# Optimization experiments

Measured on AMD Instinct MI355X. Metric: run time of the kernel, lower is better.

Reference implementation:

```python
import jax, jax.numpy as jnp
from jax import lax
import numpy as np

MS = 128            # local_map_size
HALF = MS // 2
B, S = 8, 64
C, H, W = 3, 1024, 1024


def setup_inputs() -> dict:
    key = jax.random.key(0)
    ks = jax.random.split(key, 48)
    r = lambda i, shape, s: jax.random.normal(ks[i], shape, jnp.float32) * s
    z = lambda *shape: jnp.zeros(shape, jnp.float32)
    o = lambda *shape: jnp.ones(shape, jnp.float32)
    return {
        "full_map": jax.random.normal(ks[0], (B, C, H, W), jnp.float32),
        "conditions": jax.random.uniform(ks[1], (B, 5), jnp.float32, 0.0, 1024.0),
        "input_seq": jax.random.uniform(ks[2], (B, S, 2), jnp.float32, 0.0, 1024.0),
        "steps_remaining": jax.random.uniform(ks[3], (B, S), jnp.float32, 0.0, 500.0),
        # LocalMapEncoder convs (OIHW) + batchnorm affine params
        "cw1": r(4, (16, 3, 3, 3), 0.2),   "cb1": z(16),  "g1": o(16),  "be1": z(16),
        "cw2": r(5, (32, 16, 3, 3), 0.1),  "cb2": z(32),  "g2": o(32),  "be2": z(32),
        "cw3": r(6, (64, 32, 3, 3), 0.07), "cb3": z(64),  "g3": o(64),  "be3": z(64),
        "cw4": r(7, (128, 64, 3, 3), 0.05),"cb4": z(128), "g4": o(128), "be4": z(128),
        "fw1": r(8, (512, 128 * 8 * 8), 0.01), "fb1": z(512),
        "fw2": r(9, (256, 512), 0.04),         "fb2": z(256),
        # ConditionEncoder (6 -> 128 -> 64)
        "ew1": r(10, (128, 6), 0.05),  "eb1": z(128),
        "ew2": r(11, (64, 128), 0.05), "eb2": z(64),
        # coord embedder (2 -> 32)
        "mw": r(12, (32, 2), 0.05), "mb": z(32),
        # 2-layer LSTM, torch gate order (i, f, g, o)
        "w_ih0": r(13, (4 * 256, 32), 0.05),  "w_hh0": r(14, (4 * 256, 256), 0.05),
        "b_ih0": z(4 * 256), "b_hh0": z(4 * 256),
        "w_ih1": r(15, (4 * 256, 256), 0.05), "w_hh1": r(16, (4 * 256, 256), 0.05),
        "b_ih1": z(4 * 256), "b_hh1": z(4 * 256),
        # context layer (256+256+64=576 -> 128 -> 64) and output (64 -> 2)
        "xw1": r(17, (128, 576), 0.04), "xb1": z(128),
        "xw2": r(18, (64, 128), 0.05),  "xb2": z(64),
        "ow": r(19, (2, 64), 0.1),      "ob": z(2),
    }


def _conv_bn_relu(x, w, b, g, be):
    # stride-2 3x3 conv, padding 1, NCHW/OIHW; BatchNorm in training mode (batch stats)
    y = lax.conv_general_dilated(x, w, (2, 2), ((1, 1), (1, 1)),
                                 dimension_numbers=("NCHW", "OIHW", "NCHW"))
    y = y + b[None, :, None, None]
    mu = y.mean((0, 2, 3), keepdims=True)
    var = y.var((0, 2, 3), keepdims=True)
    y = (y - mu) * lax.rsqrt(var + 1e-5) * g[None, :, None, None] + be[None, :, None, None]
    return jax.nn.relu(y)


def _lstm_layer(x, w_ih, w_hh, b_ih, b_hh):
    # x: [B, S, D] -> hidden states [B, S, Hd]
    bsz, hd = x.shape[0], w_hh.shape[1]
    bias = b_ih + b_hh
    def step(carry, xt):
        h, c = carry
        zg = xt @ w_ih.T + h @ w_hh.T + bias
        i, f, gg, oo = jnp.split(zg, 4, axis=-1)
        c = jax.nn.sigmoid(f) * c + jax.nn.sigmoid(i) * jnp.tanh(gg)
        h = jax.nn.sigmoid(oo) * jnp.tanh(c)
        return (h, c), h
    h0 = jnp.zeros((bsz, hd), x.dtype)
    _, hs = lax.scan(step, (h0, h0), x.transpose(1, 0, 2))
    return hs.transpose(1, 0, 2)


def reference(full_map, conditions, input_seq, steps_remaining,
              cw1, cb1, g1, be1, cw2, cb2, g2, be2,
              cw3, cb3, g3, be3, cw4, cb4, g4, be4,
              fw1, fb1, fw2, fb2, ew1, eb1, ew2, eb2, mw, mb,
              w_ih0, w_hh0, b_ih0, b_hh0, w_ih1, w_hh1, b_ih1, b_hh1,
              xw1, xb1, xw2, xb2, ow, ob):
    bsz, seq, _ = input_seq.shape
    # --- batched crop+pad gather (replaces host numpy loop): zero-pad map by
    # HALF on each side, then every crop is a dynamic_slice of size MS at (y, x).
    padded = jnp.pad(full_map, ((0, 0), (0, 0), (HALF, HALF), (HALF, HALF)))
    ys = input_seq[..., 0].astype(jnp.int32).reshape(-1)
    xs = input_seq[..., 1].astype(jnp.int32).reshape(-1)
    bidx = jnp.repeat(jnp.arange(bsz, dtype=jnp.int32), seq)
    crop_one = lambda b, y, x: lax.dynamic_slice(padded, (b, 0, y, x), (1, C, MS, MS))[0]
    crops = jax.vmap(crop_one)(bidx, ys, xs)              # [B*S, C, MS, MS]
    # --- LocalMapEncoder
    h = _conv_bn_relu(crops, cw1, cb1, g1, be1)
    h = _conv_bn_relu(h, cw2, cb2, g2, be2)
    h = _conv_bn_relu(h, cw3, cb3, g3, be3)
    h = _conv_bn_relu(h, cw4, cb4, g4, be4)               # [B*S, 128, 8, 8]
    h = h.reshape(h.shape[0], -1)
    h = jax.nn.relu(h @ fw1.T + fb1) @ fw2.T + fb2
    map_features = h.reshape(bsz, seq, -1)                # [B, S, 256]
    # --- ConditionEncoder on [conditions ++ steps_remaining]
    enh = jnp.concatenate(
        [jnp.broadcast_to(conditions[:, None, :], (bsz, seq, 5)),
         steps_remaining[..., None]], axis=-1)            # [B, S, 6]
    cond_features = jax.nn.relu(enh @ ew1.T + eb1) @ ew2.T + eb2  # [B, S, 64]
    # --- route predictor
    emb = jax.nn.relu(input_seq @ mw.T + mb)              # [B, S, 32]
    lstm_out = _lstm_layer(emb, w_ih0, w_hh0, b_ih0, b_hh0)
    lstm_out = _lstm_layer(lstm_out, w_ih1, w_hh1, b_ih1, b_hh1)  # [B, S, 256]
    combined = jnp.concatenate([lstm_out, map_features, cond_features], axis=-1)
    ctx = jax.nn.relu(jax.nn.relu(combined @ xw1.T + xb1) @ xw2.T + xb2)
    return ctx @ ow.T + ob                                # [B, S, 2]
```

## Files before the change

### kernel.cpp

```cpp
#include <hip/hip_runtime.h>

#define TPB 256
#define NLB 64

typedef float f32x4 __attribute__((ext_vector_type(4)));
typedef short bf16x8 __attribute__((ext_vector_type(8)));
typedef unsigned long long u64;

__device__ __forceinline__ float bf2f(unsigned short u) {
  union { unsigned int i; float f; } x; x.i = ((unsigned int)u) << 16; return x.f;
}
__device__ __forceinline__ unsigned short f2bf(float v) {
  union { float f; unsigned int i; } x; x.f = v;
  unsigned int r = (x.i + 0x7fffu + ((x.i >> 16) & 1u)) >> 16;
  return (unsigned short)r;
}
__device__ __forceinline__ float sigf(float x) { return 1.f / (1.f + __expf(-x)); }
__device__ __forceinline__ bf16x8 lda_bf8(const unsigned short* p) {
  union { uint4 u; bf16x8 v; } t; t.u = *(const uint4*)p; return t.v;
}
__device__ __forceinline__ bf16x8 frag_of(const unsigned int* w) {
  union { unsigned int u[4]; bf16x8 v; } t;
  t.u[0] = w[0]; t.u[1] = w[1]; t.u[2] = w[2]; t.u[3] = w[3]; return t.v;
}
__device__ __forceinline__ uint4 bnpack(uint4 v, const float* sst) {
  unsigned int d[4] = {v.x, v.y, v.z, v.w};
  uint4 o; unsigned int* op = (unsigned int*)&o;
#pragma unroll
  for (int t = 0; t < 4; ++t) {
    float a = fmaxf(fmaf(bf2f((unsigned short)(d[t] & 0xffff)), sst[4 * t], sst[4 * t + 1]), 0.f);
    float b = fmaxf(fmaf(bf2f((unsigned short)(d[t] >> 16)), sst[4 * t + 2], sst[4 * t + 3]), 0.f);
    op[t] = (unsigned int)f2bf(a) | ((unsigned int)f2bf(b) << 16);
  }
  return o;
}

__device__ void lstm_seg(int blkid, int p0, int p1, int first,
    const float* __restrict__ iseq, const float* __restrict__ mw, const float* __restrict__ mb,
    const float* __restrict__ w_ih0, const float* __restrict__ w_hh0,
    const float* __restrict__ b_ih0, const float* __restrict__ b_hh0,
    const float* __restrict__ w_ih1, const float* __restrict__ w_hh1,
    const float* __restrict__ b_ih1, const float* __restrict__ b_hh1,
    u64* __restrict__ h0x, u64* __restrict__ h1x,
    float* __restrict__ comb, float* __restrict__ xzg, float* __restrict__ cst,
    char* sm) {
  const int tid = threadIdx.x;
  const int u0 = blkid * 4;
  float (*xz)[8][16] = (float (*)[8][16])sm;
  char* reg2 = sm + 32768;
  float* bias1s = (float*)(sm + 51712);

  float (*embc)[8][32] = (float (*)[8][32])reg2;
  float* mwmb = (float*)(reg2 + 16384);
  unsigned short (*v0s)[264] = (unsigned short (*)[264])reg2;
  unsigned short (*w1h)[264] = (unsigned short (*)[264])(reg2 + 8448);
  float (*P0)[16]  = (float (*)[16])(reg2 + 16896);
  float (*P1a)[16] = (float (*)[16])(reg2 + 17408);
  float (*P1b)[16] = (float (*)[16])(reg2 + 17920);

  const int wv = tid >> 6, lane = tid & 63, fr = lane & 15, kg = lane >> 4;
  const int r = tid & 15, ks = tid >> 4;
  const int R  = (r >> 2) * 256 + u0 + (r & 3);
  const int Rf = (fr >> 2) * 256 + u0 + (fr & 3);

  unsigned int wfrag[8][4];
  {
    const float* wsrc = (wv == 0) ? w_hh0 : (wv == 1) ? w_ih1 : w_hh1;
#pragma unroll
    for (int ch = 0; ch < 8; ++ch)
#pragma unroll
      for (int d = 0; d < 4; ++d) {
        float lo = wsrc[(size_t)Rf * 256 + ch * 32 + kg * 8 + d * 2];
        float hi = wsrc[(size_t)Rf * 256 + ch * 32 + kg * 8 + d * 2 + 1];
        wfrag[ch][d] = (unsigned)f2bf(lo) | ((unsigned)f2bf(hi) << 16);
      }
  }
  if (tid < 16) bias1s[tid] = b_ih1[R] + b_hh1[R];

  if (first) {
    float wtmp[32];
#pragma unroll
    for (int i = 0; i < 32; ++i) wtmp[i] = w_ih0[R * 32 + i];
    const float bias0r = b_ih0[R] + b_hh0[R];
    if (tid < 96) mwmb[tid] = (tid < 64) ? mw[tid] : mb[tid - 64];
    __syncthreads();
    for (int chunk = 0; chunk < 4; ++chunk) {
      if (tid < 128) {
        int pp = tid >> 3, b = tid & 7;
        int pg = chunk * 16 + pp;
        float s0 = iseq[(b * 64 + pg) * 2 + 0];
        float s1 = iseq[(b * 64 + pg) * 2 + 1];
        for (int k = 0; k < 32; ++k)
          embc[pp][b][k] = fmaxf(fmaf(mwmb[2 * k], s0, fmaf(mwmb[2 * k + 1], s1, mwmb[64 + k])), 0.f);
      }
      __syncthreads();
      {
        int pg = chunk * 16 + ks;
        for (int b = 0; b < 8; ++b) {
          float a = bias0r;
          const float* e = &embc[ks][b][0];
#pragma unroll
          for (int k = 0; k < 32; ++k) a = fmaf(wtmp[k], e[k], a);
          xz[pg][b][r] = a;
        }
      }
      __syncthreads();
    }
    for (int i = tid; i < 8192; i += TPB)
      xzg[(size_t)blkid * 8192 + i] = ((float*)xz)[i];
  } else {
    __syncthreads();
    for (int i = tid; i < 8192; i += TPB)
      ((float*)xz)[i] = xzg[(size_t)blkid * 8192 + i];
  }
  __syncthreads();

  for (int i = tid; i < 8 * 264; i += TPB) {
    v0s[8 + i / 264][i % 264] = 0;
    w1h[8 + i / 264][i % 264] = 0;
  }
  float c0 = 0.f, c1 = 0.f;
  if (!first) {
    if (tid < 32) c0 = cst[blkid * 64 + tid];
    else if (tid < 64) c1 = cst[blkid * 64 + tid];
  }
  __syncthreads();

  for (int p = p0; p < p1; ++p) {
    if (tid < 128) {
      if (p >= 1) {
        const unsigned tag0 = (unsigned)p;
        const u64* s0p = &h0x[(size_t)(p - 1) * 1024 + tid * 8];
        u64 e[8];
        for (;;) {
          bool ok = true;
#pragma unroll
          for (int i = 0; i < 8; ++i) {
            e[i] = __hip_atomic_load(&s0p[i], __ATOMIC_RELAXED, __HIP_MEMORY_SCOPE_AGENT);
            ok &= ((unsigned)(e[i] >> 32) == tag0);
          }
          if (ok) break;
          __builtin_amdgcn_s_sleep(1);
        }
#pragma unroll
        for (int i = 0; i < 8; ++i) {
          int g = tid * 8 + i;
          int bb = (g >> 1) & 7, ub = (g >> 4) * 4 + (g & 1) * 2;
          *(unsigned int*)&v0s[bb][ub] = (unsigned int)e[i];
        }
      } else {
#pragma unroll
        for (int i = 0; i < 8; ++i) {
          int g = tid * 8 + i;
          int bb = (g >> 1) & 7, ub = (g >> 4) * 4 + (g & 1) * 2;
          *(unsigned int*)&v0s[bb][ub] = 0u;
        }
      }
    } else {
      int t2 = tid - 128;
      if (p >= 2) {
        const unsigned tag1 = (unsigned)(p - 1);
        const u64* s1p = &h1x[(size_t)(p - 2) * 1024 + t2 * 8];
        u64 e[8];
        for (;;) {
          bool ok = true;
#pragma unroll
          for (int i = 0; i < 8; ++i) {
            e[i] = __hip_atomic_load(&s1p[i], __ATOMIC_RELAXED, __HIP_MEMORY_SCOPE_AGENT);
            ok &= ((unsigned)(e[i] >> 32) == tag1);
          }
          if (ok) break;
          __builtin_amdgcn_s_sleep(1);
        }
#pragma unroll
        for (int i = 0; i < 8; ++i) {
          int g = t2 * 8 + i;
          int bb = (g >> 1) & 7, ub = (g >> 4) * 4 + (g & 1) * 2;
          *(unsigned int*)&w1h[bb][ub] = (unsigned int)e[i];
        }
      } else {
#pragma unroll
        for (int i = 0; i < 8; ++i) {
          int g = t2 * 8 + i;
          int bb = (g >> 1) & 7, ub = (g >> 4) * 4 + (g & 1) * 2;
          *(unsigned int*)&w1h[bb][ub] = 0u;
        }
      }
    }
    __syncthreads();

    if (wv == 0) {
      if (p < 64) {
        f32x4 acc = {0.f, 0.f, 0.f, 0.f};
#pragma unroll
        for (int ch = 0; ch < 8; ++ch) {
          bf16x8 af = lda_bf8(&v0s[fr][ch * 32 + kg * 8]);
          acc = __builtin_amdgcn_mfma_f32_16x16x32_bf16(af, frag_of(wfrag[ch]), acc, 0, 0, 0);
        }
#pragma unroll
        for (int j = 0; j < 4; ++j) {
          int bb2 = (lane >> 4) * 4 + j;
          if (bb2 < 8) P0[bb2][fr] = acc[j];
        }
      }
    } else if (wv == 1) {
      if (p >= 1) {
        f32x4 acc = {0.f, 0.f, 0.f, 0.f};
#pragma unroll
        for (int ch = 0; ch < 8; ++ch) {
          bf16x8 af = lda_bf8(&v0s[fr][ch * 32 + kg * 8]);
          acc = __builtin_amdgcn_mfma_f32_16x16x32_bf16(af, frag_of(wfrag[ch]), acc, 0, 0, 0);
        }
#pragma unroll
        for (int j = 0; j < 4; ++j) {
          int bb2 = (lane >> 4) * 4 + j;
          if (bb2 < 8) P1a[bb2][fr] = acc[j];
        }
      }
    } else if (wv == 2) {
      if (p >= 1) {
        f32x4 acc = {0.f, 0.f, 0.f, 0.f};
#pragma unroll
        for (int ch = 0; ch < 8; ++ch) {
          bf16x8 af = lda_bf8(&w1h[fr][ch * 32 + kg * 8]);
          acc = __builtin_amdgcn_mfma_f32_16x16x32_bf16(af, frag_of(wfrag[ch]), acc, 0, 0, 0);
        }
#pragma unroll
        for (int j = 0; j < 4; ++j) {
          int bb2 = (lane >> 4) * 4 + j;
          if (bb2 < 8) P1b[bb2][fr] = acc[j];
        }
      }
    }
    __syncthreads();

    if (tid < 32 && p < 64) {
      int b = tid >> 2, uu = tid & 3;
      float zi = P0[b][uu]      + xz[p][b][uu];
      float zf = P0[b][4 + uu]  + xz[p][b][4 + uu];
      float zg = P0[b][8 + uu]  + xz[p][b][8 + uu];
      float zo = P0[b][12 + uu] + xz[p][b][12 + uu];
      c0 = sigf(zf) * c0 + sigf(zi) * tanhf(zg);
      float h = sigf(zo) * tanhf(c0);
      float hp = __shfl_xor(h, 1);
      if (!(uu & 1)) {
        unsigned int d = (unsigned int)f2bf(h) | ((unsigned int)f2bf(hp) << 16);
        u64 v = ((u64)(unsigned)(p + 1) << 32) | d;
        __hip_atomic_store(&h0x[(size_t)p * 1024 + blkid * 16 + b * 2 + (uu >> 1)], v,
                           __ATOMIC_RELAXED, __HIP_MEMORY_SCOPE_AGENT);
      }
    } else if (tid >= 32 && tid < 64 && p >= 1) {
      int t2 = tid - 32, b = t2 >> 2, uu = t2 & 3;
      float zi = P1a[b][uu]      + P1b[b][uu]      + bias1s[uu];
      float zf = P1a[b][4 + uu]  + P1b[b][4 + uu]  + bias1s[4 + uu];
      float zg = P1a[b][8 + uu]  + P1b[b][8 + uu]  + bias1s[8 + uu];
      float zo = P1a[b][12 + uu] + P1b[b][12 + uu] + bias1s[12 + uu];
      c1 = sigf(zf) * c1 + sigf(zi) * tanhf(zg);
      float h = sigf(zo) * tanhf(c1);
      comb[(size_t)(b * 64 + (p - 1)) * 576 + u0 + uu] = h;
      float hp = __shfl_xor(h, 1);
      if (!(uu & 1)) {
        unsigned int d = (unsigned int)f2bf(h) | ((unsigned int)f2bf(hp) << 16);
        u64 v = ((u64)(unsigned)p << 32) | d;
        __hip_atomic_store(&h1x[(size_t)(p - 1) * 1024 + blkid * 16 + b * 2 + (uu >> 1)], v,
                           __ATOMIC_RELAXED, __HIP_MEMORY_SCOPE_AGENT);
      }
    }
  }

  if (tid < 32) cst[blkid * 64 + tid] = c0;
  else if (tid < 64) cst[blkid * 64 + tid] = c1;
}

#define LSTM_ARGS const float* __restrict__ iseq_l, const float* __restrict__ mw, const float* __restrict__ mb, \
    const float* __restrict__ w_ih0, const float* __restrict__ w_hh0, \
    const float* __restrict__ b_ih0, const float* __restrict__ b_hh0, \
    const float* __restrict__ w_ih1, const float* __restrict__ w_hh1, \
    const float* __restrict__ b_ih1, const float* __restrict__ b_hh1, \
    u64* __restrict__ h0x, u64* __restrict__ h1x, float* __restrict__ comb, \
    float* __restrict__ xzg, float* __restrict__ cst, int p0, int p1, int first
#define LSTM_PASS(blk) lstm_seg(blk, p0, p1, first, iseq_l, mw, mb, w_ih0, w_hh0, b_ih0, b_hh0, \
    w_ih1, w_hh1, b_ih1, b_hh1, h0x, h1x, comb, xzg, cst, sm)

__global__ __launch_bounds__(TPB, 2) void k_conv1(
    const float* __restrict__ fmap, const float* __restrict__ iseq,
    const unsigned short* __restrict__ wT, const float* __restrict__ bias,
    unsigned short* __restrict__ out, float* __restrict__ part, LSTM_ARGS) {
  __shared__ __align__(16) char sm[52288];
  const int tid = threadIdx.x;
  if (blockIdx.x < NLB) { LSTM_PASS(blockIdx.x); return; }
  const int bidc = blockIdx.x - NLB;
  unsigned short (*patch)[132][8] = (unsigned short (*)[132][8])sm;
  unsigned short (*Bsm)[104] = (unsigned short (*)[104])(sm + 35904);
  float* bs = (float*)(sm + 39232);
  float* swsum = (float*)(sm + 39296);
  float* swsq  = (float*)(sm + 39552);

  const int n = bidc >> 3, R0 = (bidc & 7) << 3;
  const int y = (int)iseq[n * 2], x = (int)iseq[n * 2 + 1];
  const int bimg = n >> 6;

  for (int e = tid; e < 1536; e += TPB) Bsm[e / 96][e % 96] = wT[e];
  if (tid < 16) bs[tid] = bias[tid];
  for (int e = tid; e < 17 * 132; e += TPB)
    *(uint4*)&patch[e / 132][e % 132][0] = uint4{0u, 0u, 0u, 0u};
  __syncthreads();
  for (int e = tid; e < 3 * 17 * 132; e += TPB) {
    int ic = e / 2244, rem = e % 2244, l = rem / 132, c = rem % 132;
    int i = 2 * R0 - 1 + l, j = c - 1;
    float v = 0.f;
    if ((unsigned)i < 128u && (unsigned)j < 128u) {
      int r = y + i - 64, cc = x + j - 64;
      if ((unsigned)r < 1024u && (unsigned)cc < 1024u)
        v = fmap[(((size_t)bimg * 3 + ic) << 20) + ((size_t)r << 10) + cc];
    }
    patch[l][c][ic] = f2bf(v);
  }
  __syncthreads();

  const int w = tid >> 6, lane = tid & 63, fr = lane & 15, kg = lane >> 4;
  f32x4 acc[8];
#pragma unroll
  for (int m = 0; m < 8; ++m) acc[m] = {0.f, 0.f, 0.f, 0.f};
#pragma unroll
  for (int ch = 0; ch < 3; ++ch) {
    int k8 = ch * 4 + kg;
    int ki = (k8 >= 9) ? 0 : ((k8 * 11) >> 5);
    int kj = (k8 >= 9) ? 0 : (k8 - 3 * ki);
    bf16x8 bfr = lda_bf8(&Bsm[fr][k8 * 8]);
#pragma unroll
    for (int m = 0; m < 8; ++m) {
      int p = w * 128 + m * 16 + fr;
      int pr = p >> 6, pc = p & 63;
      bf16x8 af = lda_bf8(&patch[2 * pr + ki][2 * pc + kj][0]);
      acc[m] = __builtin_amdgcn_mfma_f32_16x16x32_bf16(af, bfr, acc[m], 0, 0, 0);
    }
  }
  const int rg = lane >> 4;
  float bb = bs[fr];
  float sps = 0.f, spq = 0.f;
#pragma unroll
  for (int m = 0; m < 8; ++m) {
#pragma unroll
    for (int r = 0; r < 4; ++r) {
      int p = w * 128 + m * 16 + rg * 4 + r;
      int pr = p >> 6, pc = p & 63;
      float v = acc[m][r] + bb;
      sps += v; spq = fmaf(v, v, spq);
      out[(((size_t)n * 64 + R0 + pr) * 64 + pc) * 16 + fr] = f2bf(v);
    }
  }
  sps += __shfl_xor(sps, 16); spq += __shfl_xor(spq, 16);
  sps += __shfl_xor(sps, 32); spq += __shfl_xor(spq, 32);
  if (lane < 16) { swsum[w * 16 + fr] = sps; swsq[w * 16 + fr] = spq; }
  __syncthreads();
  if (tid < 16) {
    float s = swsum[tid] + swsum[16 + tid] + swsum[32 + tid] + swsum[48 + tid];
    float q = swsq[tid] + swsq[16 + tid] + swsq[32 + tid] + swsq[48 + tid];
    part[(size_t)bidc * 32 + tid * 2] = s;
    part[(size_t)bidc * 32 + tid * 2 + 1] = q;
  }
}

template<int CIN, int CB, int NS, int HIN, int HOUT>
__global__ __launch_bounds__(TPB, 2) void k_conv(
    const unsigned short* __restrict__ inb, const float* __restrict__ ssx,
    const unsigned short* __restrict__ wT, const float* __restrict__ bias,
    unsigned short* __restrict__ out, float* __restrict__ part, LSTM_ARGS) {
  constexpr int K = CIN * 9;
  constexpr int K8 = K / 8;
  constexpr int NCH = (K8 + 3) / 4;
  constexpr int KPAD = NCH * 32;
  constexpr int BS = KPAD + 8;
  constexpr int CINP = CIN + 8;
  constexpr int ICG_SH = (CIN == 16) ? 1 : (CIN == 32) ? 2 : 3;
  constexpr int TPR = HOUT / 8;
  constexpr int NT = CB / 16;
  constexpr int COUT_TOT = CB * NS;
  constexpr int PB = 289 * CINP * 2;
  constexpr int BB = CB * BS * 2;
  constexpr int CONVSM = PB + BB + CIN * 8 + CB * 32;
  constexpr int SMSZ = CONVSM > 52288 ? CONVSM : 52288;
  __shared__ __align__(16) char sm[SMSZ];
  const int tid = threadIdx.x;
  if (blockIdx.x < NLB) { LSTM_PASS(blockIdx.x); return; }
  const int bidc = blockIdx.x - NLB;

  unsigned short* patch = (unsigned short*)sm;
  unsigned short* Bsm = (unsigned short*)(sm + PB);
  float* ssl = (float*)(sm + PB + BB);
  float* swsum = (float*)(sm + PB + BB + CIN * 8);
  float* swsq = swsum + 4 * CB;

  const int n = bidc / ((TPR * TPR) * NS);
  const int rem = bidc % ((TPR * TPR) * NS);
  const int tile = rem / NS;
  const int split = rem % NS;
  const int TR0 = (tile / TPR) * 8, TC0 = (tile % TPR) * 8;
  const int oc0 = split * CB;

  for (int i = tid; i < CIN * 2; i += TPB) ssl[i] = ssx[i];
  __syncthreads();

  for (int e = tid; e < 289 * (CIN / 8); e += TPB) {
    int icg = e % (CIN / 8), pix = e / (CIN / 8);
    int row = pix / 17, col = pix % 17;
    int ir = 2 * TR0 - 1 + row, jc = 2 * TC0 - 1 + col;
    uint4 o = {0u, 0u, 0u, 0u};
    if ((unsigned)ir < (unsigned)HIN && (unsigned)jc < (unsigned)HIN) {
      uint4 v = *(const uint4*)&inb[(((size_t)n * HIN + ir) * HIN + jc) * CIN + icg * 8];
      unsigned int d[4] = {v.x, v.y, v.z, v.w};
      unsigned int* op = (unsigned int*)&o;
#pragma unroll
      for (int t = 0; t < 4; ++t) {
        int c = icg * 8 + 2 * t;
        float a = fmaxf(fmaf(bf2f((unsigned short)(d[t] & 0xffff)), ssl[2 * c], ssl[2 * c + 1]), 0.f);
        float b = fmaxf(fmaf(bf2f((unsigned short)(d[t] >> 16)), ssl[2 * c + 2], ssl[2 * c + 3]), 0.f);
        op[t] = (unsigned int)f2bf(a) | ((unsigned int)f2bf(b) << 16);
      }
    }
    *(uint4*)&patch[pix * CINP + icg * 8] = o;
  }
  for (int e = tid; e < CB * (KPAD / 8); e += TPB) {
    int oc = e / (KPAD / 8), k8i = e % (KPAD / 8);
    uint4 v = {0u, 0u, 0u, 0u};
    if (k8i * 8 < K) v = *(const uint4*)&wT[(size_t)(oc0 + oc) * K + k8i * 8];
    *(uint4*)&Bsm[oc * BS + k8i * 8] = v;
  }
  __syncthreads();

  const int wave = tid >> 6, lane = tid & 63;
  const int fr = lane & 15, kg = lane >> 4;
  const int p = wave * 16 + fr;
  const int pr = p >> 3, pc = p & 7;
  f32x4 acc[NT];
#pragma unroll
  for (int j = 0; j < NT; ++j) acc[j] = {0.f, 0.f, 0.f, 0.f};

#pragma unroll
  for (int ch = 0; ch < NCH; ++ch) {
    int k8 = ch * 4 + kg;
    int tap = k8 >> ICG_SH, icg = k8 & ((1 << ICG_SH) - 1);
    int ki = (tap * 11) >> 5;
    int kj = tap - 3 * ki;
    int addr = ((2 * pr + ki) * 17 + (2 * pc + kj)) * CINP + icg * 8;
    if (tap >= 9) addr = 0;
    bf16x8 af = lda_bf8(&patch[addr]);
#pragma unroll
    for (int j = 0; j < NT; ++j) {
      bf16x8 bfr = lda_bf8(&Bsm[(j * 16 + fr) * BS + ch * 32 + kg * 8]);
      acc[j] = __builtin_amdgcn_mfma_f32_16x16x32_bf16(af, bfr, acc[j], 0, 0, 0);
    }
  }
  const int rg = lane >> 4;
#pragma unroll
  for (int j = 0; j < NT; ++j) {
    int oc = oc0 + j * 16 + fr;
    float bb = bias[oc];
    float s1 = 0.f, q1 = 0.f;
#pragma unroll
    for (int r = 0; r < 4; ++r) {
      int pp = wave * 16 + rg * 4 + r;
      int orow = TR0 + (pp >> 3), ocol = TC0 + (pp & 7);
      float v = acc[j][r] + bb;
      s1 += v; q1 = fmaf(v, v, q1);
      out[(((size_t)n * HOUT + orow) * HOUT + ocol) * COUT_TOT + oc] = f2bf(v);
    }
    s1 += __shfl_xor(s1, 16); q1 += __shfl_xor(q1, 16);
    s1 += __shfl_xor(s1, 32); q1 += __shfl_xor(q1, 32);
    if (lane < 16) { swsum[wave * CB + j * 16 + fr] = s1; swsq[wave * CB + j * 16 + fr] = q1; }
  }
  __syncthreads();
  if (tid < CB) {
    float s = swsum[tid] + swsum[CB + tid] + swsum[2 * CB + tid] + swsum[3 * CB + tid];
    float q = swsq[tid] + swsq[CB + tid] + swsq[2 * CB + tid] + swsq[3 * CB + tid];
    part[(size_t)bidc * CB * 2 + tid * 2] = s;
    part[(size_t)bidc * CB * 2 + tid * 2 + 1] = q;
  }
}

__global__ __launch_bounds__(TPB, 2) void k_fc1(
    const unsigned short* __restrict__ A, const unsigned short* __restrict__ W,
    const float* __restrict__ ssx, const float* __restrict__ bias, float* __restrict__ out,
    LSTM_ARGS) {
  __shared__ __align__(16) char sm[52288];
  const int tid = threadIdx.x;
  if (blockIdx.x < NLB) { LSTM_PASS(blockIdx.x); return; }
  const int cid = blockIdx.x - NLB;
  const int bm = (cid >> 3) * 64, bn = (cid & 7) * 64;

  unsigned short (*As)[64] = (unsigned short (*)[64])sm;
  unsigned short (*Bs)[64] = (unsigned short (*)[64])(sm + 8192);
  float* ssl = (float*)(sm + 16384);
  const int lane = tid & 63, wave = tid >> 6;
  const int wr = (wave >> 1) * 32, wc = (wave & 1) * 32;
  f32x4 acc00 = {0.f, 0.f, 0.f, 0.f}, acc01 = acc00, acc10 = acc00, acc11 = acc00;
  const int r0 = tid >> 3, c0 = tid & 7;
  const int fr = lane & 15, kg = lane >> 4;
  for (int i = tid; i < 256; i += TPB) ssl[i] = ssx[i];
  __syncthreads();
  for (int kt = 0; kt < 128; ++kt) {
    const int kb = kt * 64;
    uint4 av0 = *(const uint4*)&A[(size_t)(bm + r0) * 8192 + kb + c0 * 8];
    uint4 av1 = *(const uint4*)&A[(size_t)(bm + r0 + 32) * 8192 + kb + c0 * 8];
    uint4 bv0 = *(const uint4*)&W[(size_t)(bn + r0) * 8192 + kb + c0 * 8];
    uint4 bv1 = *(const uint4*)&W[(size_t)(bn + r0 + 32) * 8192 + kb + c0 * 8];
    const float* sst = &ssl[2 * ((kb + c0 * 8) & 127)];
    __syncthreads();
    av0 = bnpack(av0, sst);
    av1 = bnpack(av1, sst);
    *(uint4*)&As[r0][(c0 ^ (r0 & 7)) * 8] = av0;
    *(uint4*)&As[r0 + 32][(c0 ^ (r0 & 7)) * 8] = av1;
    *(uint4*)&Bs[r0][(c0 ^ (r0 & 7)) * 8] = bv0;
    *(uint4*)&Bs[r0 + 32][(c0 ^ (r0 & 7)) * 8] = bv1;
    __syncthreads();
#pragma unroll
    for (int ks = 0; ks < 2; ++ks) {
      int ch = ks * 4 + kg;
      int ra0 = wr + fr, ra1 = wr + 16 + fr;
      int rb0 = wc + fr, rb1 = wc + 16 + fr;
      bf16x8 a_0 = lda_bf8(&As[ra0][(ch ^ (ra0 & 7)) * 8]);
      bf16x8 a_1 = lda_bf8(&As[ra1][(ch ^ (ra1 & 7)) * 8]);
      bf16x8 b_0 = lda_bf8(&Bs[rb0][(ch ^ (rb0 & 7)) * 8]);
      bf16x8 b_1 = lda_bf8(&Bs[rb1][(ch ^ (rb1 & 7)) * 8]);
      acc00 = __builtin_amdgcn_mfma_f32_16x16x32_bf16(a_0, b_0, acc00, 0, 0, 0);
      acc01 = __builtin_amdgcn_mfma_f32_16x16x32_bf16(a_0, b_1, acc01, 0, 0, 0);
      acc10 = __builtin_amdgcn_mfma_f32_16x16x32_bf16(a_1, b_0, acc10, 0, 0, 0);
      acc11 = __builtin_amdgcn_mfma_f32_16x16x32_bf16(a_1, b_1, acc11, 0, 0, 0);
    }
  }
  const int rg = lane >> 4;
  int n0 = bn + wc + fr, n1 = n0 + 16;
  float bi0 = bias[n0], bi1 = bias[n1];
#pragma unroll
  for (int r = 0; r < 4; ++r) {
    int m0 = bm + wr + rg * 4 + r, m1 = m0 + 16;
    out[m0 * 512 + n0] = fmaxf(acc00[r] + bi0, 0.f);
    out[m0 * 512 + n1] = fmaxf(acc01[r] + bi1, 0.f);
    out[m1 * 512 + n0] = fmaxf(acc10[r] + bi0, 0.f);
    out[m1 * 512 + n1] = fmaxf(acc11[r] + bi1, 0.f);
  }
}

__global__ __launch_bounds__(TPB) void stats_final3(const float* __restrict__ part,
    const float* __restrict__ gamma, const float* __restrict__ beta,
    float* __restrict__ ss, float inv_count, int COUT_BLK, int NSPLIT, int NBID) {
  const int c = blockIdx.x, tid = threadIdx.x;
  const int split = c / COUT_BLK, loc = c % COUT_BLK;
  const int NG = NBID / NSPLIT;
  float s = 0.f, q = 0.f;
  for (int g = tid; g < NG; g += TPB) {
    size_t b = (size_t)g * NSPLIT + split;
    s += part[b * COUT_BLK * 2 + loc * 2];
    q += part[b * COUT_BLK * 2 + loc * 2 + 1];
  }
  __shared__ float rs[TPB], rq[TPB];
  rs[tid] = s; rq[tid] = q;
  __syncthreads();
  for (int off = TPB / 2; off > 0; off >>= 1) {
    if (tid < off) { rs[tid] += rs[tid + off]; rq[tid] += rq[tid + off]; }
    __syncthreads();
  }
  if (tid == 0) {
    float mean = rs[0] * inv_count;
    float var  = rq[0] * inv_count - mean * mean;
    float rstd = rsqrtf(var + 1e-5f);
    float scl  = gamma[c] * rstd;
    ss[2 * c] = scl;
    ss[2 * c + 1] = beta[c] - mean * scl;
  }
}

__global__ __launch_bounds__(TPB) void prep_wt(
    const float* __restrict__ w1, const float* __restrict__ w2,
    const float* __restrict__ w3, const float* __restrict__ w4,
    unsigned short* __restrict__ wt1, unsigned short* __restrict__ wt2,
    unsigned short* __restrict__ wt3, unsigned short* __restrict__ wt4) {
  int i = blockIdx.x * TPB + threadIdx.x;
  if (i < 1536) {
    int oc = i / 96, k = i % 96;
    int tap = k >> 3, ic = k & 7;
    float v = (tap < 9 && ic < 3) ? w1[(oc * 3 + ic) * 9 + tap] : 0.f;
    wt1[i] = f2bf(v);
  } else if (i < 6144) {
    int j = i - 1536;
    int oc = j / 144, k = j % 144;
    wt2[j] = f2bf(w2[(oc * 16 + (k & 15)) * 9 + (k >> 4)]);
  } else if (i < 24576) {
    int j = i - 6144;
    int oc = j / 288, k = j % 288;
    wt3[j] = f2bf(w3[(oc * 32 + (k & 31)) * 9 + (k >> 5)]);
  } else if (i < 98304) {
    int j = i - 24576;
    int oc = j / 576, k = j % 576;
    wt4[j] = f2bf(w4[(oc * 64 + (k & 63)) * 9 + (k >> 6)]);
  }
}

__global__ __launch_bounds__(TPB) void permute_fw1(const float* __restrict__ in,
    unsigned short* __restrict__ out) {
  __shared__ unsigned short l[128 * 66];
  int n = blockIdx.x;
  for (int e = threadIdx.x; e < 8192; e += TPB) {
    int c = e >> 6, pix = e & 63;
    l[c * 66 + pix] = f2bf(in[(size_t)n * 8192 + e]);
  }
  __syncthreads();
  for (int e = threadIdx.x; e < 8192; e += TPB) {
    int pix = e >> 7, c = e & 127;
    out[(size_t)n * 8192 + e] = l[c * 66 + pix];
  }
}

__global__ __launch_bounds__(TPB, 2) void gemm_m64(
    const float* __restrict__ A, const float* __restrict__ W,
    const float* __restrict__ bias, float* __restrict__ out,
    int N, int K, int relu, int ldo, int coff) {
  __shared__ unsigned short As[64 * 40];
  __shared__ unsigned short Bs[64 * 40];
  const int tid = threadIdx.x, lane = tid & 63, wave = tid >> 6;
  const int wr = (wave >> 1) * 32, wc = (wave & 1) * 32;
  const int bm = blockIdx.y * 64, bn = blockIdx.x * 64;
  const int fr = lane & 15, kg = lane >> 4;
  const int sr = tid >> 2, sc = (tid & 3) * 8;
  f32x4 a00 = {0.f, 0.f, 0.f, 0.f}, a01 = a00, a10 = a00, a11 = a00;
  int nch = (K + 31) >> 5;
  for (int ch = 0; ch < nch; ++ch) {
    int kb = ch * 32;
    __syncthreads();
    {
      unsigned short tmp[8];
#pragma unroll
      for (int j = 0; j < 8; ++j) {
        int k = kb + sc + j;
        tmp[j] = (k < K) ? f2bf(A[(size_t)(bm + sr) * K + k]) : (unsigned short)0;
      }
      *(uint4*)&As[sr * 40 + sc] = *(const uint4*)tmp;
      int wrow = bn + sr;
#pragma unroll
      for (int j = 0; j < 8; ++j) {
        int k = kb + sc + j;
        tmp[j] = (wrow < N && k < K) ? f2bf(W[(size_t)wrow * K + k]) : (unsigned short)0;
      }
      *(uint4*)&Bs[sr * 40 + sc] = *(const uint4*)tmp;
    }
    __syncthreads();
    bf16x8 af0 = lda_bf8(&As[(wr + fr) * 40 + kg * 8]);
    bf16x8 af1 = lda_bf8(&As[(wr + 16 + fr) * 40 + kg * 8]);
    bf16x8 bf0 = lda_bf8(&Bs[(wc + fr) * 40 + kg * 8]);
    bf16x8 bf1 = lda_bf8(&Bs[(wc + 16 + fr) * 40 + kg * 8]);
    a00 = __builtin_amdgcn_mfma_f32_16x16x32_bf16(af0, bf0, a00, 0, 0, 0);
    a01 = __builtin_amdgcn_mfma_f32_16x16x32_bf16(af0, bf1, a01, 0, 0, 0);
    a10 = __builtin_amdgcn_mfma_f32_16x16x32_bf16(af1, bf0, a10, 0, 0, 0);
    a11 = __builtin_amdgcn_mfma_f32_16x16x32_bf16(af1, bf1, a11, 0, 0, 0);
  }
  const int rg = lane >> 4;
  int n0 = bn + wc + fr, n1 = n0 + 16;
  float bi0 = (n0 < N) ? bias[n0] : 0.f;
  float bi1 = (n1 < N) ? bias[n1] : 0.f;
#pragma unroll
  for (int r = 0; r < 4; ++r) {
    int m0 = bm + wr + rg * 4 + r, m1 = m0 + 16;
    if (n0 < N) {
      float v = a00[r] + bi0; out[(size_t)m0 * ldo + coff + n0] = relu ? fmaxf(v, 0.f) : v;
      v = a10[r] + bi0;       out[(size_t)m1 * ldo + coff + n0] = relu ? fmaxf(v, 0.f) : v;
    }
    if (n1 < N) {
      float v = a01[r] + bi1; out[(size_t)m0 * ldo + coff + n1] = relu ? fmaxf(v, 0.f) : v;
      v = a11[r] + bi1;       out[(size_t)m1 * ldo + coff + n1] = relu ? fmaxf(v, 0.f) : v;
    }
  }
}

__global__ __launch_bounds__(TPB) void cond_enc(
    const float* __restrict__ cond, const float* __restrict__ steps,
    const float* __restrict__ ew1, const float* __restrict__ eb1,
    const float* __restrict__ ew2, const float* __restrict__ eb2,
    float* __restrict__ comb) {
  __shared__ float w1s[128][8];
  __shared__ float w2s[64][132];
  __shared__ float hbuf[64][132];
  const int tid = threadIdx.x;
  const int row0 = blockIdx.x * 64;
  for (int e = tid; e < 128 * 8; e += TPB) {
    int k = e >> 3, t = e & 7;
    w1s[k][t] = (t < 6) ? ew1[k * 6 + t] : (t == 6 ? eb1[k] : 0.f);
  }
  for (int e = tid; e < 64 * 128; e += TPB) {
    int j = e >> 7, k = e & 127;
    w2s[j][k] = ew2[j * 128 + k];
  }
  __syncthreads();
  {
    int row = tid >> 2, ks = tid & 3;
    int n = row0 + row;
    int b = n >> 6, s = n & 63;
    float e0 = cond[b * 5], e1 = cond[b * 5 + 1], e2 = cond[b * 5 + 2];
    float e3 = cond[b * 5 + 3], e4 = cond[b * 5 + 4];
    float e5 = steps[b * 64 + s];
    for (int k = ks * 32; k < ks * 32 + 32; ++k) {
      float a = fmaf(w1s[k][0], e0, fmaf(w1s[k][1], e1, fmaf(w1s[k][2], e2,
                fmaf(w1s[k][3], e3, fmaf(w1s[k][4], e4, fmaf(w1s[k][5], e5, w1s[k][6]))))));
      hbuf[row][k] = fmaxf(a, 0.f);
    }
  }
  __syncthreads();
  {
    int row = tid >> 2, js = tid & 3;
    int n = row0 + row;
    for (int j = js * 16; j < js * 16 + 16; ++j) {
      float a = eb2[j];
#pragma unroll 8
      for (int k = 0; k < 128; ++k) a = fmaf(w2s[j][k], hbuf[row][k], a);
      comb[(size_t)n * 576 + 512 + j] = a;
    }
  }
}

extern "C" void kernel_launch(void* const* d_in, const int* in_sizes, int n_in,
                              void* d_out, int out_size, void* d_ws, size_t ws_size,
                              hipStream_t stream) {
  const float* fmap  = (const float*)d_in[0];
  const float* cond  = (const float*)d_in[1];
  const float* iseq  = (const float*)d_in[2];
  const float* steps = (const float*)d_in[3];
  const float* cw1 = (const float*)d_in[4];  const float* cb1 = (const float*)d_in[5];
  const float* g1  = (const float*)d_in[6];  const float* be1 = (const float*)d_in[7];
  const float* cw2 = (const float*)d_in[8];  const float* cb2 = (const float*)d_in[9];
  const float* g2  = (const float*)d_in[10]; const float* be2 = (const float*)d_in[11];
  const float* cw3 = (const float*)d_in[12]; const float* cb3 = (const float*)d_in[13];
  const float* g3  = (const float*)d_in[14]; const float* be3 = (const float*)d_in[15];
  const float* cw4 = (const float*)d_in[16]; const float* cb4 = (const float*)d_in[17];
  const float* g4  = (const float*)d_in[18]; const float* be4 = (const float*)d_in[19];
  const float* fw1 = (const float*)d_in[20]; const float* fb1 = (const float*)d_in[21];
  const float* fw2 = (const float*)d_in[22]; const float* fb2 = (const float*)d_in[23];
  const float* ew1 = (const float*)d_in[24]; const float* eb1 = (const float*)d_in[25];
  const float* ew2 = (const float*)d_in[26]; const float* eb2 = (const float*)d_in[27];
  const float* mw  = (const float*)d_in[28]; const float* mb  = (const float*)d_in[29];
  const float* w_ih0 = (const float*)d_in[30]; const float* w_hh0 = (const float*)d_in[31];
  const float* b_ih0 = (const float*)d_in[32]; const float* b_hh0 = (const float*)d_in[33];
  const float* w_ih1 = (const float*)d_in[34]; const float* w_hh1 = (const float*)d_in[35];
  const float* b_ih1 = (const float*)d_in[36]; const float* b_hh1 = (const float*)d_in[37];
  const float* xw1 = (const float*)d_in[38]; const float* xb1 = (const float*)d_in[39];
  const float* xw2 = (const float*)d_in[40]; const float* xb2 = (const float*)d_in[41];
  const float* ow  = (const float*)d_in[42]; const float* ob  = (const float*)d_in[43];

  float* ws = (float*)d_ws;
  unsigned short* y1bf  = (unsigned short*)ws;
  unsigned short* y2bf  = (unsigned short*)(ws + 16777216);
  unsigned short* y3bf  = (unsigned short*)(ws + 25165824);
  unsigned short* y4pre = (unsigned short*)(ws + 29360128);
  unsigned short* fw1bf = (unsigned short*)(ws + 33554432);
  size_t base = 35651584;
  float* part  = ws + base; base += 524288;
  float* ss1   = ws + base; base += 32;
  float* ss2   = ws + base; base += 64;
  float* ss3   = ws + base; base += 128;
  float* ss4   = ws + base; base += 256;
  float* f1    = ws + base; base += 262144;
  u64*   h0x   = (u64*)(ws + base); base += 131072;
  u64*   h1x   = (u64*)(ws + base); base += 131072;
  float* comb  = ws + base; base += 294912;
  float* cx1   = ws + base; base += 65536;
  float* cx2   = ws + base; base += 32768;
  unsigned short* wt1 = (unsigned short*)(ws + base); base += 768;
  unsigned short* wt2 = (unsigned short*)(ws + base); base += 2304;
  unsigned short* wt3 = (unsigned short*)(ws + base); base += 9216;
  unsigned short* wt4 = (unsigned short*)(ws + base); base += 36864;
  float* xzg = ws + base; base += 524288;
  float* cst = ws + base; base += 4096;

  prep_wt<<<384, TPB, 0, stream>>>(cw1, cw2, cw3, cw4, wt1, wt2, wt3, wt4);
  permute_fw1<<<512, TPB, 0, stream>>>(fw1, fw1bf);
  hipMemsetAsync(h0x, 0, 2 * 64 * 1024 * sizeof(u64), stream);

  k_conv1<<<NLB + 4096, TPB, 0, stream>>>(fmap, iseq, wt1, cb1, y1bf, part,
      iseq, mw, mb, w_ih0, w_hh0, b_ih0, b_hh0, w_ih1, w_hh1, b_ih1, b_hh1,
      h0x, h1x, comb, xzg, cst, 0, 24, 1);
  stats_final3<<<16, TPB, 0, stream>>>(part, g1, be1, ss1, 1.f / 2097152.f, 16, 1, 4096);
  k_conv<16, 32, 1, 64, 32><<<NLB + 8192, TPB, 0, stream>>>(y1bf, ss1, wt2, cb2, y2bf, part,
      iseq, mw, mb, w_ih0, w_hh0, b_ih0, b_hh0, w_ih1, w_hh1, b_ih1, b_hh1,
      h0x, h1x, comb, xzg, cst, 24, 38, 0);
  stats_final3<<<32, TPB, 0, stream>>>(part, g2, be2, ss2, 1.f / 524288.f, 32, 1, 8192);
  k_conv<32, 64, 1, 32, 16><<<NLB + 2048, TPB, 0, stream>>>(y2bf, ss2, wt3, cb3, y3bf, part,
      iseq, mw, mb, w_ih0, w_hh0, b_ih0, b_hh0, w_ih1, w_hh1, b_ih1, b_hh1,
      h0x, h1x, comb, xzg, cst, 38, 45, 0);
  stats_final3<<<64, TPB, 0, stream>>>(part, g3, be3, ss3, 1.f / 131072.f, 64, 1, 2048);
  k_conv<64, 32, 4, 16, 8><<<NLB + 2048, TPB, 0, stream>>>(y3bf, ss3, wt4, cb4, y4pre, part,
      iseq, mw, mb, w_ih0, w_hh0, b_ih0, b_hh0, w_ih1, w_hh1, b_ih1, b_hh1,
      h0x, h1x, comb, xzg, cst, 45, 52, 0);
  stats_final3<<<128, TPB, 0, stream>>>(part, g4, be4, ss4, 1.f / 32768.f, 32, 4, 2048);
  k_fc1<<<NLB + 64, TPB, 0, stream>>>(y4pre, fw1bf, ss4, fb1, f1,
      iseq, mw, mb, w_ih0, w_hh0, b_ih0, b_hh0, w_ih1, w_hh1, b_ih1, b_hh1,
      h0x, h1x, comb, xzg, cst, 52, 65, 0);

  gemm_m64<<<dim3(4, 8), TPB, 0, stream>>>(f1, fw2, fb2, comb, 256, 512, 0, 576, 256);
  cond_enc<<<8, TPB, 0, stream>>>(cond, steps, ew1, eb1, ew2, eb2, comb);

  gemm_m64<<<dim3(2, 8), TPB, 0, stream>>>(comb, xw1, xb1, cx1, 128, 576, 1, 128, 0);
  gemm_m64<<<dim3(1, 8), TPB, 0, stream>>>(cx1, xw2, xb2, cx2, 64, 128, 1, 64, 0);
  gemm_m64<<<dim3(1, 8), TPB, 0, stream>>>(cx2, ow, ob, (float*)d_out, 2, 64, 0, 2, 0);
}
```

Measured before the change: 592.5 us.

## Pre-cast full map to bf16 and move LSTM segments out of conv1

Adds a cast_map kernel that converts the whole fp32 full_map to bf16 before conv1, so conv1 gathers half-size elements and skips per-element conversion. conv1 no longer hosts the persistent LSTM blocks; it uses static shared memory and allows four blocks per CU. The LSTM step ranges are redistributed across the later conv and fc1 launches. The cast reads and writes the entire 100MB map, far more than the crops touch, so it adds substantial bandwidth cost.

Measured after the change: 663.8 us. 12.0% more time.

```diff
diff --git a/kernel.cpp b/kernel.cpp
--- a/kernel.cpp
+++ b/kernel.cpp
@@ -282,20 +282,26 @@
 #define LSTM_PASS(blk) lstm_seg(blk, p0, p1, first, iseq_l, mw, mb, w_ih0, w_hh0, b_ih0, b_hh0, \
     w_ih1, w_hh1, b_ih1, b_hh1, h0x, h1x, comb, xzg, cst, sm)
 
-__global__ __launch_bounds__(TPB, 2) void k_conv1(
-    const float* __restrict__ fmap, const float* __restrict__ iseq,
+__global__ __launch_bounds__(TPB) void cast_map(const float* __restrict__ in,
+    unsigned short* __restrict__ out, int nquad) {
+  for (int q = blockIdx.x * TPB + threadIdx.x; q < nquad; q += gridDim.x * TPB) {
+    float4 v = ((const float4*)in)[q];
+    ushort4 o;
+    o.x = f2bf(v.x); o.y = f2bf(v.y); o.z = f2bf(v.z); o.w = f2bf(v.w);
+    ((ushort4*)out)[q] = o;
+  }
+}
+
+__global__ __launch_bounds__(TPB, 4) void k_conv1(
+    const unsigned short* __restrict__ fmapbf, const float* __restrict__ iseq,
     const unsigned short* __restrict__ wT, const float* __restrict__ bias,
-    unsigned short* __restrict__ out, float* __restrict__ part, LSTM_ARGS) {
-  __shared__ __align__(16) char sm[52288];
+    unsigned short* __restrict__ out, float* __restrict__ part) {
+  __shared__ __align__(16) unsigned short patch[17][132][8];
+  __shared__ unsigned short Bsm[16][104];
+  __shared__ float bs[16];
+  __shared__ float swsum[64], swsq[64];
   const int tid = threadIdx.x;
-  if (blockIdx.x < NLB) { LSTM_PASS(blockIdx.x); return; }
-  const int bidc = blockIdx.x - NLB;
-  unsigned short (*patch)[132][8] = (unsigned short (*)[132][8])sm;
-  unsigned short (*Bsm)[104] = (unsigned short (*)[104])(sm + 35904);
-  float* bs = (float*)(sm + 39232);
-  float* swsum = (float*)(sm + 39296);
-  float* swsq  = (float*)(sm + 39552);
-
+  const int bidc = blockIdx.x;
   const int n = bidc >> 3, R0 = (bidc & 7) << 3;
   const int y = (int)iseq[n * 2], x = (int)iseq[n * 2 + 1];
   const int bimg = n >> 6;
@@ -308,13 +314,13 @@
   for (int e = tid; e < 3 * 17 * 132; e += TPB) {
     int ic = e / 2244, rem = e % 2244, l = rem / 132, c = rem % 132;
     int i = 2 * R0 - 1 + l, j = c - 1;
-    float v = 0.f;
+    unsigned short v = 0;
     if ((unsigned)i < 128u && (unsigned)j < 128u) {
       int r = y + i - 64, cc = x + j - 64;
       if ((unsigned)r < 1024u && (unsigned)cc < 1024u)
-        v = fmap[(((size_t)bimg * 3 + ic) << 20) + ((size_t)r << 10) + cc];
-    }
-    patch[l][c][ic] = f2bf(v);
+        v = fmapbf[(((size_t)bimg * 3 + ic) << 20) + ((size_t)r << 10) + cc];
+    }
+    patch[l][c][ic] = v;
   }
   __syncthreads();
 
@@ -769,30 +775,30 @@
   unsigned short* wt4 = (unsigned short*)(ws + base); base += 36864;
   float* xzg = ws + base; base += 524288;
   float* cst = ws + base; base += 4096;
+  unsigned short* fmapbf = (unsigned short*)(ws + base); base += 12582912;
 
   prep_wt<<<384, TPB, 0, stream>>>(cw1, cw2, cw3, cw4, wt1, wt2, wt3, wt4);
   permute_fw1<<<512, TPB, 0, stream>>>(fw1, fw1bf);
+  cast_map<<<4096, TPB, 0, stream>>>(fmap, fmapbf, 6291456);
   hipMemsetAsync(h0x, 0, 2 * 64 * 1024 * sizeof(u64), stream);
 
-  k_conv1<<<NLB + 4096, TPB, 0, stream>>>(fmap, iseq, wt1, cb1, y1bf, part,
-      iseq, mw, mb, w_ih0, w_hh0, b_ih0, b_hh0, w_ih1, w_hh1, b_ih1, b_hh1,
-      h0x, h1x, comb, xzg, cst, 0, 24, 1);
+  k_conv1<<<4096, TPB, 0, stream>>>(fmapbf, iseq, wt1, cb1, y1bf, part);
   stats_final3<<<16, TPB, 0, stream>>>(part, g1, be1, ss1, 1.f / 2097152.f, 16, 1, 4096);
   k_conv<16, 32, 1, 64, 32><<<NLB + 8192, TPB, 0, stream>>>(y1bf, ss1, wt2, cb2, y2bf, part,
       iseq, mw, mb, w_ih0, w_hh0, b_ih0, b_hh0, w_ih1, w_hh1, b_ih1, b_hh1,
-      h0x, h1x, comb, xzg, cst, 24, 38, 0);
+      h0x, h1x, comb, xzg, cst, 0, 26, 1);
   stats_final3<<<32, TPB, 0, stream>>>(part, g2, be2, ss2, 1.f / 524288.f, 32, 1, 8192);
   k_conv<32, 64, 1, 32, 16><<<NLB + 2048, TPB, 0, stream>>>(y2bf, ss2, wt3, cb3, y3bf, part,
       iseq, mw, mb, w_ih0, w_hh0, b_ih0, b_hh0, w_ih1, w_hh1, b_ih1, b_hh1,
-      h0x, h1x, comb, xzg, cst, 38, 45, 0);
+      h0x, h1x, comb, xzg, cst, 26, 40, 0);
   stats_final3<<<64, TPB, 0, stream>>>(part, g3, be3, ss3, 1.f / 131072.f, 64, 1, 2048);
   k_conv<64, 32, 4, 16, 8><<<NLB + 2048, TPB, 0, stream>>>(y3bf, ss3, wt4, cb4, y4pre, part,
       iseq, mw, mb, w_ih0, w_hh0, b_ih0, b_hh0, w_ih1, w_hh1, b_ih1, b_hh1,
-      h0x, h1x, comb, xzg, cst, 45, 52, 0);
+      h0x, h1x, comb, xzg, cst, 40, 54, 0);
   stats_final3<<<128, TPB, 0, stream>>>(part, g4, be4, ss4, 1.f / 32768.f, 32, 4, 2048);
   k_fc1<<<NLB + 64, TPB, 0, stream>>>(y4pre, fw1bf, ss4, fb1, f1,
       iseq, mw, mb, w_ih0, w_hh0, b_ih0, b_hh0, w_ih1, w_hh1, b_ih1, b_hh1,
-      h0x, h1x, comb, xzg, cst, 52, 65, 0);
+      h0x, h1x, comb, xzg, cst, 54, 65, 0);
 
   gemm_m64<<<dim3(4, 8), TPB, 0, stream>>>(f1, fw2, fb2, comb, 256, 512, 0, 576, 256);
   cond_enc<<<8, TPB, 0, stream>>>(cond, steps, ew1, eb1, ew2, eb2, comb);
```
